# Kernel optimization log

Hardware: AMD Instinct MI355X
Metric: run time of the kernel (lower is better)

## Reference

```python
import jax, jax.numpy as jnp
import numpy as np

B, S, D, H = 2, 2048, 1024, 16
D_H = D // H  # 64


def setup_inputs() -> dict:
    key = jax.random.key(0)
    ks = jax.random.split(key, 12)
    inp = {
        "query": jax.random.normal(ks[0], (B, S, D), dtype=jnp.float32),
        "key":   jax.random.normal(ks[1], (B, S, D), dtype=jnp.float32),
        "value": jax.random.normal(ks[2], (B, S, D), dtype=jnp.float32),
        # causal 0/1 float mask, broadcastable to [B, H, Sq, Sk]; 1 = masked
        "mask":  jnp.broadcast_to(jnp.triu(jnp.ones((S, S), dtype=jnp.float32), k=1)[None, None], (B, 1, S, S)),
    }
    scale = 0.02
    inp["wq"] = jax.random.normal(ks[3], (D, D), dtype=jnp.float32) * scale
    inp["bq"] = jnp.zeros((D,), dtype=jnp.float32)
    inp["wk"] = jax.random.normal(ks[4], (D, D), dtype=jnp.float32) * scale
    inp["bk"] = jnp.zeros((D,), dtype=jnp.float32)
    inp["wv"] = jax.random.normal(ks[5], (D, D), dtype=jnp.float32) * scale
    inp["bv"] = jnp.zeros((D,), dtype=jnp.float32)
    inp["wff"] = jax.random.normal(ks[6], (D, D), dtype=jnp.float32) * scale
    inp["bff"] = jnp.zeros((D,), dtype=jnp.float32)
    return inp


def _split_head(x):
    # [B, S, D] -> [B, H, S, d_h]
    b, s, _ = x.shape
    return x.reshape(b, s, H, D_H).transpose(0, 2, 1, 3)


def reference(query, key, value, mask, wq, bq, wk, bk, wv, bv, wff, bff):
    # QKV projections (torch Linear: x @ W.T + b)
    q = _split_head(query @ wq.T + bq)
    k = _split_head(key @ wk.T + bk)
    v = _split_head(value @ wv.T + bv)
    # scaled dot-product attention
    scores = jnp.einsum("bhqd,bhkd->bhqk", q, k) / jnp.sqrt(jnp.float32(D_H))
    scores = scores + mask * (-1e9)
    attn = jax.nn.softmax(scores, axis=-1)
    out = jnp.einsum("bhqk,bhkd->bhqd", attn, v)
    # concat heads: [B, H, S, d_h] -> [B, S, D]
    out = out.transpose(0, 2, 1, 3).reshape(query.shape[0], query.shape[1], D)
    return out @ wff.T + bff
```

## Files before the change

### kernel.cpp

```cpp
#include <hip/hip_runtime.h>
#include <hip/hip_bf16.h>

#define B_  2
#define S_  2048
#define D_  1024
#define H_  16
#define DH_ 64
#define M_  (B_ * S_)

using bf16x8 = __attribute__((ext_vector_type(8))) short;
using s16x4  = __attribute__((ext_vector_type(4))) short;
using f32x4  = __attribute__((ext_vector_type(4))) float;

__device__ __forceinline__ bf16x8 ldg8(const __hip_bfloat16* p) {
    bf16x8 v;
    __builtin_memcpy(&v, p, 16);
    return v;
}
__device__ __forceinline__ bf16x8 lds8(const void* p) {
    bf16x8 v;
    __builtin_memcpy(&v, p, 16);
    return v;
}
__device__ __forceinline__ f32x4 lds4f(const void* p) {
    f32x4 v;
    __builtin_memcpy(&v, p, 16);
    return v;
}
__device__ __forceinline__ void gll16(const void* g, void* l) {
    __builtin_amdgcn_global_load_lds(
        (const __attribute__((address_space(1))) unsigned int*)g,
        (__attribute__((address_space(3))) unsigned int*)l,
        16, 0, 0);
}
__device__ __forceinline__ short bf16bits(float x) {
    __hip_bfloat16 hv = __float2bfloat16(x);
    short sv;
    __builtin_memcpy(&sv, &hv, 2);
    return sv;
}
__device__ __forceinline__ unsigned cvtpk(float lo, float hi) {
    unsigned r;
    asm("v_cvt_pk_bf16_f32 %0, %1, %2" : "=v"(r) : "v"(lo), "v"(hi));
    return r;
}

__global__ void cvt_w(const float* __restrict__ wq, const float* __restrict__ wk,
                      const float* __restrict__ wv, const float* __restrict__ wff,
                      __hip_bfloat16* __restrict__ Wq, __hip_bfloat16* __restrict__ Wk,
                      __hip_bfloat16* __restrict__ Wv, __hip_bfloat16* __restrict__ Wf) {
    const size_t e = (size_t)(blockIdx.x * 256 + threadIdx.x) * 8;
    const int i = (int)(e >> 20);
    const size_t off = e & (((size_t)1 << 20) - 1);
    const float* src = (i == 0) ? wq : (i == 1) ? wk : (i == 2) ? wv : wff;
    __hip_bfloat16* dst = (i == 0) ? Wq : (i == 1) ? Wk : (i == 2) ? Wv : Wf;
    float4 a, b;
    __builtin_memcpy(&a, src + off, 16);
    __builtin_memcpy(&b, src + off + 4, 16);
    __hip_bfloat16 h[8];
    h[0] = __float2bfloat16(a.x); h[1] = __float2bfloat16(a.y);
    h[2] = __float2bfloat16(a.z); h[3] = __float2bfloat16(a.w);
    h[4] = __float2bfloat16(b.x); h[5] = __float2bfloat16(b.y);
    h[6] = __float2bfloat16(b.z); h[7] = __float2bfloat16(b.w);
    __builtin_memcpy(dst + off, h, 16);
}

template<int MI, bool AF32>
__device__ __forceinline__
void gemm_body(const void* __restrict__ Ap,
               const __hip_bfloat16* __restrict__ W,
               const float* __restrict__ bias,
               void* __restrict__ out, int mode, float oscale,
               int row0, int col0) {
    constexpr int K  = D_;
    constexpr int N  = D_;
    constexpr int TM = MI * 32;
    constexpr int AB = AF32 ? 128 : 64;
    __shared__ __align__(16) char At[2][TM][AB];
    __shared__ __hip_bfloat16 Wt[2][128][32];

    const int tid = threadIdx.x;
    const int w   = tid >> 6;
    const int l   = tid & 63;
    const int lr  = l & 15;
    const int lg  = l >> 4;
    const int wr  = (w >> 1) * (MI * 16);
    const int wc  = (w & 1) * 64;

    const int srow4  = l >> 2;
    const int schk4  = l & 3;
    const int srow8  = l >> 3;
    const int schk8  = l & 7;

    f32x4 acc[MI][4] = {};

    auto STAGE = [&](int buf, int k0) {
        if (AF32) {
#pragma unroll
            for (int r = 0; r < TM / 32; ++r) {
                const int row = r * 32 + w * 8 + srow8;
                const int csw = (schk8 ^ (row & 7)) * 4;
                gll16((const float*)Ap + (size_t)(row0 + row) * K + k0 + csw,
                      &At[buf][r * 32 + w * 8][0]);
            }
        } else {
#pragma unroll
            for (int r = 0; r < TM / 64; ++r) {
                const int row = r * 64 + w * 16 + srow4;
                const int csw = (schk4 ^ (row & 3)) * 8;
                gll16((const __hip_bfloat16*)Ap + (size_t)(row0 + row) * K + k0 + csw,
                      &At[buf][r * 64 + w * 16][0]);
            }
        }
#pragma unroll
        for (int r = 0; r < 2; ++r) {
            const int row = r * 64 + w * 16 + srow4;
            const int csw = (schk4 ^ (row & 3)) * 8;
            gll16(W + (size_t)(col0 + row) * K + k0 + csw, &Wt[buf][r * 64 + w * 16][0]);
        }
    };

    STAGE(0, 0);
    int cur = 0;
    for (int k0 = 0; k0 < K; k0 += 32) {
        __syncthreads();
        if (k0 + 32 < K) STAGE(cur ^ 1, k0 + 32);
        bf16x8 af[MI], wf[4];
#pragma unroll
        for (int m = 0; m < MI; ++m) {
            const int arow = wr + m * 16 + lr;
            if (AF32) {
                const int c0 = (2 * lg) ^ (arow & 7);
                const int c1 = (2 * lg + 1) ^ (arow & 7);
                f32x4 a0 = lds4f(&At[cur][arow][c0 * 16]);
                f32x4 a1 = lds4f(&At[cur][arow][c1 * 16]);
                unsigned uu[4] = { cvtpk(a0[0], a0[1]), cvtpk(a0[2], a0[3]),
                                   cvtpk(a1[0], a1[1]), cvtpk(a1[2], a1[3]) };
                __builtin_memcpy(&af[m], uu, 16);
            } else {
                af[m] = lds8(&At[cur][arow][((lg ^ (arow & 3)) * 8) * 2]);
            }
        }
#pragma unroll
        for (int n = 0; n < 4; ++n) {
            const int wrow = wc + n * 16 + lr;
            wf[n] = lds8(&Wt[cur][wrow][(lg ^ (wrow & 3)) * 8]);
        }
#pragma unroll
        for (int m = 0; m < MI; ++m)
#pragma unroll
            for (int n = 0; n < 4; ++n)
                acc[m][n] = __builtin_amdgcn_mfma_f32_16x16x32_bf16(
                    af[m], wf[n], acc[m][n], 0, 0, 0);
        cur ^= 1;
    }

    float bv[4];
#pragma unroll
    for (int n = 0; n < 4; ++n) bv[n] = bias[col0 + wc + n * 16 + lr];

    if (mode == 1) {
#pragma unroll
        for (int m = 0; m < MI; ++m) {
            const int row_s = row0 + wr + m * 16 + lg * 4;
            const int bq = row_s >> 11, s0 = row_s & (S_ - 1);
#pragma unroll
            for (int n = 0; n < 4; ++n) {
                const int col = col0 + wc + n * 16 + lr;
                const int h = col >> 6, d = col & (DH_ - 1);
                s16x4 pk;
#pragma unroll
                for (int r = 0; r < 4; ++r) pk[r] = bf16bits(acc[m][n][r] + bv[n]);
                __builtin_memcpy(
                    (__hip_bfloat16*)out + ((size_t)((bq * H_ + h) * DH_) + d) * S_ + s0,
                    &pk, 8);
            }
        }
    } else {
#pragma unroll
        for (int m = 0; m < MI; ++m)
#pragma unroll
            for (int n = 0; n < 4; ++n)
#pragma unroll
                for (int r = 0; r < 4; ++r) {
                    const int row = row0 + wr + m * 16 + lg * 4 + r;
                    const int col = col0 + wc + n * 16 + lr;
                    const float v = acc[m][n][r] + bv[n];
                    if (mode == 0)
                        ((__hip_bfloat16*)out)[(size_t)row * N + col] =
                            __float2bfloat16(v * oscale);
                    else
                        ((float*)out)[(size_t)row * N + col] = v;
                }
    }
}

__global__ __launch_bounds__(256)
void gemm_qkv(const float* __restrict__ Xq, const float* __restrict__ Xk,
              const float* __restrict__ Xv, const __hip_bfloat16* __restrict__ Wq,
              const __hip_bfloat16* __restrict__ Wk, const __hip_bfloat16* __restrict__ Wv,
              const float* __restrict__ bq, const float* __restrict__ bk,
              const float* __restrict__ bv,
              __hip_bfloat16* __restrict__ Qp, __hip_bfloat16* __restrict__ Kp,
              __hip_bfloat16* __restrict__ Vt) {
    const int z = blockIdx.z;
    const void* A           = (z == 0) ? (const void*)Xq : (z == 1) ? (const void*)Xk : (const void*)Xv;
    const __hip_bfloat16* W = (z == 0) ? Wq : (z == 1) ? Wk : Wv;
    const float* bias       = (z == 0) ? bq : (z == 1) ? bk : bv;
    void* out               = (z == 0) ? (void*)Qp : (z == 1) ? (void*)Kp : (void*)Vt;
    const float osc = (z == 0) ? 0.125f * 1.4426950408889634f : 1.f;

    const int lin  = blockIdx.y * 8 + blockIdx.x;
    const int xcd  = lin & 7;
    const int idx  = lin >> 3;
    const int row0 = (xcd * 4 + (idx & 3)) * 128;
    const int col0 = (idx >> 2) * 128;

    gemm_body<4, true>(A, W, bias, out, (z == 2) ? 1 : 0, osc, row0, col0);
}

__global__ __launch_bounds__(256)
void gemm_ff(const __hip_bfloat16* __restrict__ A, const __hip_bfloat16* __restrict__ W,
             const float* __restrict__ bias, float* __restrict__ out) {
    const int lin  = blockIdx.y * 8 + blockIdx.x;
    const int xcd  = lin & 7;
    const int idx  = lin >> 3;
    const int row0 = (xcd * 8 + (idx & 7)) * 64;
    const int col0 = (idx >> 3) * 128;
    gemm_body<2, false>(A, W, bias, out, 2, 1.f, row0, col0);
}

__global__ __launch_bounds__(512)
void attn_fwd(const __hip_bfloat16* __restrict__ Qp,
              const __hip_bfloat16* __restrict__ Kp,
              const __hip_bfloat16* __restrict__ Vt,
              __hip_bfloat16* __restrict__ O) {
    __shared__ __hip_bfloat16 Kt[2][64][64];
    __shared__ __hip_bfloat16 Vs[2][64][64];
    __shared__ __hip_bfloat16 Pl[8][16][64];

    const int tid = threadIdx.x;
    const int w   = tid >> 6;
    const int l   = tid & 63;
    const int lr  = l & 15;
    const int lg  = l >> 4;

    const int raw = blockIdx.x;
    const int wg  = (raw & 7) * 64 + (raw >> 3);
    const int xcd = wg >> 6;
    const int loc = wg & 63;
    const int bhi = loc >> 4;
    const int prr = loc & 15;
    const int pr  = (bhi >= 2) ? (15 - prr) : prr;
    const int bh  = xcd * 4 + bhi;
    const int h   = bh & (H_ - 1);
    const int b   = bh >> 4;

    const int sub  = w >> 2;
    const int qb_s = sub ? (31 - pr) : pr;
    const int qw0  = qb_s * 64 + (w & 3) * 16;

    bf16x8 aq[2];
#pragma unroll
    for (int kc = 0; kc < 2; ++kc)
        aq[kc] = ldg8(Qp + (size_t)(b * S_ + qw0 + lr) * D_ + h * DH_ + kc * 32 + lg * 8);

    f32x4 o[4] = {};
    f32x4 rs4 = {};

    const int nkt_max = 32 - pr;

    const int srow   = l >> 3;
    const int schunk = l & 7;
    const int psw    = (lr & 7) << 4;

    auto STAGE = [&](int buf, int kt) {
        const int k0 = kt * 64;
        const int row = w * 8 + srow;
        const int csw = (schunk ^ (row & 7)) * 8;
        gll16(Kp + (size_t)(b * S_ + k0 + row) * D_ + h * DH_ + csw,
              &Kt[buf][w * 8][0]);
        gll16(Vt + ((size_t)((b * H_ + h) * DH_) + row) * S_ + k0 + csw,
              &Vs[buf][w * 8][0]);
    };

    char* prow = (char*)&Pl[w][lr][0];

    auto STEP = [&](int kt, int cur) {
        const int k0 = kt * 64;
        __syncthreads();
        if (kt + 1 < nkt_max) STAGE(cur ^ 1, kt + 1);

        if (kt <= qb_s) {
            f32x4 sc[4] = {};
            __builtin_amdgcn_s_setprio(1);
#pragma unroll
            for (int kk = 0; kk < 4; ++kk) {
                const int krow = kk * 16 + lr;
#pragma unroll
                for (int kc = 0; kc < 2; ++kc) {
                    bf16x8 kf = lds8(&Kt[cur][krow][((kc * 4 + lg) ^ (krow & 7)) * 8]);
                    sc[kk] = __builtin_amdgcn_mfma_f32_16x16x32_bf16(kf, aq[kc], sc[kk], 0, 0, 0);
                }
            }
            __builtin_amdgcn_s_setprio(0);

            const int qrow = qw0 + lr;
            if (kt == qb_s) {
#pragma unroll
                for (int kk = 0; kk < 4; ++kk) {
                    float pv[4];
#pragma unroll
                    for (int r = 0; r < 4; ++r) {
                        const int key = k0 + kk * 16 + lg * 4 + r;
                        pv[r] = (key > qrow) ? 0.f : exp2f(sc[kk][r]);
                        rs4[r] += pv[r];
                    }
                    unsigned uu[2] = { cvtpk(pv[0], pv[1]), cvtpk(pv[2], pv[3]) };
                    __builtin_memcpy(prow + ((kk * 32 + lg * 8) ^ psw), uu, 8);
                }
            } else {
#pragma unroll
                for (int kk = 0; kk < 4; ++kk) {
                    float pv[4];
#pragma unroll
                    for (int r = 0; r < 4; ++r) {
                        pv[r] = exp2f(sc[kk][r]);
                        rs4[r] += pv[r];
                    }
                    unsigned uu[2] = { cvtpk(pv[0], pv[1]), cvtpk(pv[2], pv[3]) };
                    __builtin_memcpy(prow + ((kk * 32 + lg * 8) ^ psw), uu, 8);
                }
            }

            bf16x8 pa[2];
#pragma unroll
            for (int kc = 0; kc < 2; ++kc)
                __builtin_memcpy(&pa[kc], prow + ((kc * 64 + lg * 16) ^ psw), 16);
            __builtin_amdgcn_s_setprio(1);
#pragma unroll
            for (int j = 0; j < 4; ++j) {
                const int vrow = j * 16 + lr;
#pragma unroll
                for (int kc = 0; kc < 2; ++kc) {
                    bf16x8 vf = lds8(&Vs[cur][vrow][((kc * 4 + lg) ^ (vrow & 7)) * 8]);
                    o[j] = __builtin_amdgcn_mfma_f32_16x16x32_bf16(pa[kc], vf, o[j], 0, 0, 0);
                }
            }
            __builtin_amdgcn_s_setprio(0);
        }
    };

    STAGE(0, 0);
    for (int kt = 0; kt < nkt_max; kt += 2) {
        STEP(kt, 0);
        if (kt + 1 < nkt_max) STEP(kt + 1, 1);
    }

    float rsf = rs4[0] + rs4[1] + rs4[2] + rs4[3];
    rsf += __shfl_xor(rsf, 16);
    rsf += __shfl_xor(rsf, 32);
#pragma unroll
    for (int r = 0; r < 4; ++r) {
        const float inv = 1.f / __shfl(rsf, 4 * lg + r);
        const int row = qw0 + 4 * lg + r;
#pragma unroll
        for (int j = 0; j < 4; ++j)
            O[((size_t)(b * S_ + row)) * D_ + h * DH_ + j * 16 + lr] =
                __float2bfloat16(o[j][r] * inv);
    }
}

extern "C" void kernel_launch(void* const* d_in, const int* in_sizes, int n_in,
                              void* d_out, int out_size, void* d_ws, size_t ws_size,
                              hipStream_t stream) {
    const float* q    = (const float*)d_in[0];
    const float* kin  = (const float*)d_in[1];
    const float* vin  = (const float*)d_in[2];
    const float* wq   = (const float*)d_in[4];
    const float* bq   = (const float*)d_in[5];
    const float* wk   = (const float*)d_in[6];
    const float* bk   = (const float*)d_in[7];
    const float* wv   = (const float*)d_in[8];
    const float* bv   = (const float*)d_in[9];
    const float* wff  = (const float*)d_in[10];
    const float* bff  = (const float*)d_in[11];

    char* ws = (char*)d_ws;
    const size_t MB = 1024 * 1024;
    __hip_bfloat16* Wqb = (__hip_bfloat16*)(ws + 24 * MB);
    __hip_bfloat16* Wkb = (__hip_bfloat16*)(ws + 26 * MB);
    __hip_bfloat16* Wvb = (__hip_bfloat16*)(ws + 28 * MB);
    __hip_bfloat16* Wfb = (__hip_bfloat16*)(ws + 30 * MB);
    __hip_bfloat16* Qp  = (__hip_bfloat16*)(ws + 32 * MB);
    __hip_bfloat16* Kp  = (__hip_bfloat16*)(ws + 40 * MB);
    __hip_bfloat16* Vt  = (__hip_bfloat16*)(ws + 48 * MB);
    __hip_bfloat16* Ob  = (__hip_bfloat16*)(ws + 56 * MB);

    cvt_w<<<2048, 256, 0, stream>>>(wq, wk, wv, wff, Wqb, Wkb, Wvb, Wfb);

    dim3 gq(8, 32, 3);
    gemm_qkv<<<gq, 256, 0, stream>>>(q, kin, vin, Wqb, Wkb, Wvb,
                                     bq, bk, bv, Qp, Kp, Vt);

    attn_fwd<<<512, 512, 0, stream>>>(Qp, Kp, Vt, Ob);

    dim3 gg(8, 64);
    gemm_ff<<<gg, 256, 0, stream>>>(Ob, Wfb, bff, (float*)d_out);
}
```

Baseline: 114.5 us.

## Balance causal attention work across warp groups with split-K on high query block

```diff
diff --git a/kernel.cpp b/kernel.cpp
--- a/kernel.cpp
+++ b/kernel.cpp
@@ -235,139 +235,164 @@
               const __hip_bfloat16* __restrict__ Kp,
               const __hip_bfloat16* __restrict__ Vt,
               __hip_bfloat16* __restrict__ O) {
-    __shared__ __hip_bfloat16 Kt[2][64][64];
-    __shared__ __hip_bfloat16 Vs[2][64][64];
-    __shared__ __hip_bfloat16 Pl[8][16][64];
+    __shared__ __hip_bfloat16 Kt[2][2][32][64];
+    __shared__ __hip_bfloat16 Vs[2][2][64][32];
+    __shared__ __hip_bfloat16 Pl[8][16][32];
 
     const int tid = threadIdx.x;
     const int w   = tid >> 6;
     const int l   = tid & 63;
     const int lr  = l & 15;
     const int lg  = l >> 4;
+    const int grp = w >> 2;
+    const int wi  = w & 3;
 
     const int raw = blockIdx.x;
     const int wg  = (raw & 7) * 64 + (raw >> 3);
-    const int xcd = wg >> 6;
-    const int loc = wg & 63;
-    const int bhi = loc >> 4;
-    const int prr = loc & 15;
-    const int pr  = (bhi >= 2) ? (15 - prr) : prr;
-    const int bh  = xcd * 4 + bhi;
+    const int bh  = wg >> 4;
+    const int pr  = wg & 15;
     const int h   = bh & (H_ - 1);
     const int b   = bh >> 4;
 
-    const int sub  = w >> 2;
-    const int qb_s = sub ? (31 - pr) : pr;
-    const int qw0  = qb_s * 64 + (w & 3) * 16;
-
-    bf16x8 aq[2];
-#pragma unroll
-    for (int kc = 0; kc < 2; ++kc)
-        aq[kc] = ldg8(Qp + (size_t)(b * S_ + qw0 + lr) * D_ + h * DH_ + kc * 32 + lg * 8);
-
-    f32x4 o[4] = {};
-    f32x4 rs4 = {};
-
-    const int nkt_max = 32 - pr;
-
-    const int srow   = l >> 3;
-    const int schunk = l & 7;
-    const int psw    = (lr & 7) << 4;
-
-    auto STAGE = [&](int buf, int kt) {
-        const int k0 = kt * 64;
-        const int row = w * 8 + srow;
-        const int csw = (schunk ^ (row & 7)) * 8;
-        gll16(Kp + (size_t)(b * S_ + k0 + row) * D_ + h * DH_ + csw,
-              &Kt[buf][w * 8][0]);
-        gll16(Vt + ((size_t)((b * H_ + h) * DH_) + row) * S_ + k0 + csw,
-              &Vs[buf][w * 8][0]);
+    const int qwL = pr * 64 + wi * 16;
+    const int qwH = (31 - pr) * 64 + wi * 16;
+    const int tL  = 2 * pr + 2;
+
+    const int psw = (lr & 3) << 4;
+
+    bf16x8 aqL[2], aqH[2];
+#pragma unroll
+    for (int kc = 0; kc < 2; ++kc) {
+        aqL[kc] = ldg8(Qp + (size_t)(b * S_ + qwL + lr) * D_ + h * DH_ + kc * 32 + lg * 8);
+        aqH[kc] = ldg8(Qp + (size_t)(b * S_ + qwH + lr) * D_ + h * DH_ + kc * 32 + lg * 8);
+    }
+
+    f32x4 oL[4] = {}, oH[4] = {};
+    f32x4 rsL4 = {}, rsH4 = {};
+
+    auto tile0 = [&](int s) { return (s < tL) ? s : (s + 31 - 2 * pr); };
+
+    auto STAGE = [&](int stream, int buf, int kt) {
+        const int k0 = kt * 32;
+        const int krow = wi * 8 + (l >> 3);
+        const int kcsw = ((l & 7) ^ (krow & 7)) * 8;
+        gll16(Kp + (size_t)(b * S_ + k0 + krow) * D_ + h * DH_ + kcsw,
+              &Kt[stream][buf][wi * 8][0]);
+        const int vrow = wi * 16 + (l >> 2);
+        const int vcsw = ((l & 3) ^ (vrow & 3)) * 8;
+        gll16(Vt + ((size_t)((b * H_ + h) * DH_) + vrow) * S_ + k0 + vcsw,
+              &Vs[stream][buf][wi * 16][0]);
     };
 
     char* prow = (char*)&Pl[w][lr][0];
 
-    auto STEP = [&](int kt, int cur) {
-        const int k0 = kt * 64;
+    auto UNIT = [&](int stream, int buf, int kt, const bf16x8 (&aq)[2],
+                    f32x4 (&o)[4], f32x4& rs4, int qw0) {
+        const int k0 = kt * 32;
+        f32x4 sc[2] = {};
+        __builtin_amdgcn_s_setprio(1);
+#pragma unroll
+        for (int kk = 0; kk < 2; ++kk) {
+            const int krow = kk * 16 + lr;
+#pragma unroll
+            for (int kc = 0; kc < 2; ++kc) {
+                bf16x8 kf = lds8(&Kt[stream][buf][krow][((kc * 4 + lg) ^ (krow & 7)) * 8]);
+                sc[kk] = __builtin_amdgcn_mfma_f32_16x16x32_bf16(kf, aq[kc], sc[kk], 0, 0, 0);
+            }
+        }
+        __builtin_amdgcn_s_setprio(0);
+
+        const int qrow = qw0 + lr;
+#pragma unroll
+        for (int kk = 0; kk < 2; ++kk) {
+            float pv[4];
+#pragma unroll
+            for (int r = 0; r < 4; ++r) {
+                const int key = k0 + kk * 16 + lg * 4 + r;
+                pv[r] = (key > qrow) ? 0.f : exp2f(sc[kk][r]);
+                rs4[r] += pv[r];
+            }
+            unsigned uu[2] = { cvtpk(pv[0], pv[1]), cvtpk(pv[2], pv[3]) };
+            __builtin_memcpy(prow + ((kk * 32 + lg * 8) ^ psw), uu, 8);
+        }
+
+        bf16x8 pa;
+        __builtin_memcpy(&pa, prow + ((lg * 16) ^ psw), 16);
+        __builtin_amdgcn_s_setprio(1);
+#pragma unroll
+        for (int j = 0; j < 4; ++j) {
+            const int vrow = j * 16 + lr;
+            bf16x8 vf = lds8(&Vs[stream][buf][vrow][(lg ^ (vrow & 3)) * 8]);
+            o[j] = __builtin_amdgcn_mfma_f32_16x16x32_bf16(pa, vf, o[j], 0, 0, 0);
+        }
+        __builtin_amdgcn_s_setprio(0);
+    };
+
+    if (grp == 0) STAGE(0, 0, tile0(0));
+    else          STAGE(1, 0, 0);
+
+    for (int s = 0; s < 33; ++s) {
+        const int buf = s & 1;
         __syncthreads();
-        if (kt + 1 < nkt_max) STAGE(cur ^ 1, kt + 1);
-
-        if (kt <= qb_s) {
-            f32x4 sc[4] = {};
-            __builtin_amdgcn_s_setprio(1);
-#pragma unroll
-            for (int kk = 0; kk < 4; ++kk) {
-                const int krow = kk * 16 + lr;
-#pragma unroll
-                for (int kc = 0; kc < 2; ++kc) {
-                    bf16x8 kf = lds8(&Kt[cur][krow][((kc * 4 + lg) ^ (krow & 7)) * 8]);
-                    sc[kk] = __builtin_amdgcn_mfma_f32_16x16x32_bf16(kf, aq[kc], sc[kk], 0, 0, 0);
-                }
-            }
-            __builtin_amdgcn_s_setprio(0);
-
-            const int qrow = qw0 + lr;
-            if (kt == qb_s) {
-#pragma unroll
-                for (int kk = 0; kk < 4; ++kk) {
-                    float pv[4];
-#pragma unroll
-                    for (int r = 0; r < 4; ++r) {
-                        const int key = k0 + kk * 16 + lg * 4 + r;
-                        pv[r] = (key > qrow) ? 0.f : exp2f(sc[kk][r]);
-                        rs4[r] += pv[r];
-                    }
-                    unsigned uu[2] = { cvtpk(pv[0], pv[1]), cvtpk(pv[2], pv[3]) };
-                    __builtin_memcpy(prow + ((kk * 32 + lg * 8) ^ psw), uu, 8);
-                }
-            } else {
-#pragma unroll
-                for (int kk = 0; kk < 4; ++kk) {
-                    float pv[4];
-#pragma unroll
-                    for (int r = 0; r < 4; ++r) {
-                        pv[r] = exp2f(sc[kk][r]);
-                        rs4[r] += pv[r];
-                    }
-                    unsigned uu[2] = { cvtpk(pv[0], pv[1]), cvtpk(pv[2], pv[3]) };
-                    __builtin_memcpy(prow + ((kk * 32 + lg * 8) ^ psw), uu, 8);
-                }
-            }
-
-            bf16x8 pa[2];
-#pragma unroll
-            for (int kc = 0; kc < 2; ++kc)
-                __builtin_memcpy(&pa[kc], prow + ((kc * 64 + lg * 16) ^ psw), 16);
-            __builtin_amdgcn_s_setprio(1);
-#pragma unroll
-            for (int j = 0; j < 4; ++j) {
-                const int vrow = j * 16 + lr;
-#pragma unroll
-                for (int kc = 0; kc < 2; ++kc) {
-                    bf16x8 vf = lds8(&Vs[cur][vrow][((kc * 4 + lg) ^ (vrow & 7)) * 8]);
-                    o[j] = __builtin_amdgcn_mfma_f32_16x16x32_bf16(pa[kc], vf, o[j], 0, 0, 0);
-                }
-            }
-            __builtin_amdgcn_s_setprio(0);
-        }
+        if (s + 1 < 33) {
+            if (grp == 0) STAGE(0, buf ^ 1, tile0(s + 1));
+            else          STAGE(1, buf ^ 1, s + 1);
+        }
+        if (grp == 0) {
+            if (s < tL) UNIT(0, buf, s, aqL, oL, rsL4, qwL);
+            else        UNIT(0, buf, s + 31 - 2 * pr, aqH, oH, rsH4, qwH);
+        } else {
+            UNIT(1, buf, s, aqH, oH, rsH4, qwH);
+        }
+    }
+
+    auto rsum = [&](const f32x4& v) {
+        float x = v[0] + v[1] + v[2] + v[3];
+        x += __shfl_xor(x, 16);
+        x += __shfl_xor(x, 32);
+        return x;
     };
 
-    STAGE(0, 0);
-    for (int kt = 0; kt < nkt_max; kt += 2) {
-        STEP(kt, 0);
-        if (kt + 1 < nkt_max) STEP(kt + 1, 1);
-    }
-
-    float rsf = rs4[0] + rs4[1] + rs4[2] + rs4[3];
-    rsf += __shfl_xor(rsf, 16);
-    rsf += __shfl_xor(rsf, 32);
-#pragma unroll
-    for (int r = 0; r < 4; ++r) {
-        const float inv = 1.f / __shfl(rsf, 4 * lg + r);
-        const int row = qw0 + 4 * lg + r;
+    float* Ox = (float*)&Kt[0][0][0][0];
+    float* Rx = (float*)&Vs[0][0][0][0];
+
+    __syncthreads();
+    if (grp == 1) {
+        const float rsf = rsum(rsH4);
 #pragma unroll
         for (int j = 0; j < 4; ++j)
-            O[((size_t)(b * S_ + row)) * D_ + h * DH_ + j * 16 + lr] =
-                __float2bfloat16(o[j][r] * inv);
+#pragma unroll
+            for (int r = 0; r < 4; ++r)
+                Ox[(wi * 16 + 4 * lg + r) * 64 + j * 16 + lr] = oH[j][r];
+        if (l < 16) Rx[wi * 16 + lr] = rsf;
+    }
+    __syncthreads();
+    if (grp == 0) {
+        const float rsfL = rsum(rsL4);
+#pragma unroll
+        for (int r = 0; r < 4; ++r) {
+            const float inv = 1.f / __shfl(rsfL, 4 * lg + r);
+            const int row = qwL + 4 * lg + r;
+#pragma unroll
+            for (int j = 0; j < 4; ++j)
+                O[((size_t)(b * S_ + row)) * D_ + h * DH_ + j * 16 + lr] =
+                    __float2bfloat16(oL[j][r] * inv);
+        }
+        const float tot = rsum(rsH4) + Rx[wi * 16 + lr];
+#pragma unroll
+        for (int j = 0; j < 4; ++j)
+#pragma unroll
+            for (int r = 0; r < 4; ++r)
+                oH[j][r] += Ox[(wi * 16 + 4 * lg + r) * 64 + j * 16 + lr];
+#pragma unroll
+        for (int r = 0; r < 4; ++r) {
+            const float inv = 1.f / __shfl(tot, 4 * lg + r);
+            const int row = qwH + 4 * lg + r;
+#pragma unroll
+            for (int j = 0; j < 4; ++j)
+                O[((size_t)(b * S_ + row)) * D_ + h * DH_ + j * 16 + lr] =
+                    __float2bfloat16(oH[j][r] * inv);
+        }
     }
 }
 
```

Result: slower. 118.9 us (+3.9%).

## Stage 128-key K/V tiles per barrier in causal attention kernel

Applied to the files above, without the earlier changes.

```diff
diff --git a/kernel.cpp b/kernel.cpp
--- a/kernel.cpp
+++ b/kernel.cpp
@@ -235,8 +235,8 @@
               const __hip_bfloat16* __restrict__ Kp,
               const __hip_bfloat16* __restrict__ Vt,
               __hip_bfloat16* __restrict__ O) {
-    __shared__ __hip_bfloat16 Kt[2][64][64];
-    __shared__ __hip_bfloat16 Vs[2][64][64];
+    __shared__ __hip_bfloat16 Kt[2][128][64];
+    __shared__ __hip_bfloat16 Vs[2][64][128];
     __shared__ __hip_bfloat16 Pl[8][16][64];
 
     const int tid = threadIdx.x;
@@ -247,12 +247,11 @@
 
     const int raw = blockIdx.x;
     const int wg  = (raw & 7) * 64 + (raw >> 3);
-    const int xcd = wg >> 6;
     const int loc = wg & 63;
     const int bhi = loc >> 4;
     const int prr = loc & 15;
     const int pr  = (bhi >= 2) ? (15 - prr) : prr;
-    const int bh  = xcd * 4 + bhi;
+    const int bh  = (wg >> 6) * 4 + bhi;
     const int h   = bh & (H_ - 1);
     const int b   = bh >> 4;
 
@@ -268,93 +267,86 @@
     f32x4 o[4] = {};
     f32x4 rs4 = {};
 
-    const int nkt_max = 32 - pr;
-
-    const int srow   = l >> 3;
-    const int schunk = l & 7;
-    const int psw    = (lr & 7) << 4;
-
-    auto STAGE = [&](int buf, int kt) {
-        const int k0 = kt * 64;
-        const int row = w * 8 + srow;
-        const int csw = (schunk ^ (row & 7)) * 8;
-        gll16(Kp + (size_t)(b * S_ + k0 + row) * D_ + h * DH_ + csw,
-              &Kt[buf][w * 8][0]);
-        gll16(Vt + ((size_t)((b * H_ + h) * DH_) + row) * S_ + k0 + csw,
-              &Vs[buf][w * 8][0]);
+    const int nt = (33 - pr) >> 1;
+    const int psw = (lr & 7) << 4;
+
+    auto STAGE = [&](int buf, int t) {
+        const int k0 = t * 128;
+#pragma unroll
+        for (int r = 0; r < 2; ++r) {
+            const int krow = w * 16 + r * 8 + (l >> 3);
+            const int kcsw = ((l & 7) ^ (krow & 7)) * 8;
+            gll16(Kp + (size_t)(b * S_ + k0 + krow) * D_ + h * DH_ + kcsw,
+                  &Kt[buf][w * 16 + r * 8][0]);
+        }
+#pragma unroll
+        for (int r = 0; r < 2; ++r) {
+            const int vrow = w * 8 + r * 4 + (l >> 4);
+            const int vcsw = ((l & 15) ^ (vrow & 15)) * 8;
+            gll16(Vt + ((size_t)((b * H_ + h) * DH_) + vrow) * S_ + k0 + vcsw,
+                  &Vs[buf][w * 8 + r * 4][0]);
+        }
     };
 
     char* prow = (char*)&Pl[w][lr][0];
 
-    auto STEP = [&](int kt, int cur) {
-        const int k0 = kt * 64;
+    auto UNIT = [&](int buf, int u, int half) {
+        const int k0 = u * 64;
+        f32x4 sc[4] = {};
+        __builtin_amdgcn_s_setprio(1);
+#pragma unroll
+        for (int kk = 0; kk < 4; ++kk) {
+            const int krow = half * 64 + kk * 16 + lr;
+#pragma unroll
+            for (int kc = 0; kc < 2; ++kc) {
+                bf16x8 kf = lds8(&Kt[buf][krow][((kc * 4 + lg) ^ (krow & 7)) * 8]);
+                sc[kk] = __builtin_amdgcn_mfma_f32_16x16x32_bf16(kf, aq[kc], sc[kk], 0, 0, 0);
+            }
+        }
+        __builtin_amdgcn_s_setprio(0);
+
+        const int qrow = qw0 + lr;
+#pragma unroll
+        for (int kk = 0; kk < 4; ++kk) {
+            float pv[4];
+#pragma unroll
+            for (int r = 0; r < 4; ++r) {
+                const int key = k0 + kk * 16 + lg * 4 + r;
+                pv[r] = (key > qrow) ? 0.f : exp2f(sc[kk][r]);
+                rs4[r] += pv[r];
+            }
+            unsigned uu[2] = { cvtpk(pv[0], pv[1]), cvtpk(pv[2], pv[3]) };
+            __builtin_memcpy(prow + ((kk * 32 + lg * 8) ^ psw), uu, 8);
+        }
+
+        bf16x8 pa[2];
+#pragma unroll
+        for (int kc = 0; kc < 2; ++kc)
+            __builtin_memcpy(&pa[kc], prow + ((kc * 64 + lg * 16) ^ psw), 16);
+        __builtin_amdgcn_s_setprio(1);
+#pragma unroll
+        for (int j = 0; j < 4; ++j) {
+            const int vrow = j * 16 + lr;
+#pragma unroll
+            for (int kc = 0; kc < 2; ++kc) {
+                const int chunk = (half * 8 + kc * 4 + lg) ^ (vrow & 15);
+                bf16x8 vf = lds8(&Vs[buf][vrow][chunk * 8]);
+                o[j] = __builtin_amdgcn_mfma_f32_16x16x32_bf16(pa[kc], vf, o[j], 0, 0, 0);
+            }
+        }
+        __builtin_amdgcn_s_setprio(0);
+    };
+
+    STAGE(0, 0);
+    for (int t = 0; t < nt; ++t) {
+        const int buf = t & 1;
         __syncthreads();
-        if (kt + 1 < nkt_max) STAGE(cur ^ 1, kt + 1);
-
-        if (kt <= qb_s) {
-            f32x4 sc[4] = {};
-            __builtin_amdgcn_s_setprio(1);
-#pragma unroll
-            for (int kk = 0; kk < 4; ++kk) {
-                const int krow = kk * 16 + lr;
-#pragma unroll
-                for (int kc = 0; kc < 2; ++kc) {
-                    bf16x8 kf = lds8(&Kt[cur][krow][((kc * 4 + lg) ^ (krow & 7)) * 8]);
-                    sc[kk] = __builtin_amdgcn_mfma_f32_16x16x32_bf16(kf, aq[kc], sc[kk], 0, 0, 0);
-                }
-            }
-            __builtin_amdgcn_s_setprio(0);
-
-            const int qrow = qw0 + lr;
-            if (kt == qb_s) {
-#pragma unroll
-                for (int kk = 0; kk < 4; ++kk) {
-                    float pv[4];
-#pragma unroll
-                    for (int r = 0; r < 4; ++r) {
-                        const int key = k0 + kk * 16 + lg * 4 + r;
-                        pv[r] = (key > qrow) ? 0.f : exp2f(sc[kk][r]);
-                        rs4[r] += pv[r];
-                    }
-                    unsigned uu[2] = { cvtpk(pv[0], pv[1]), cvtpk(pv[2], pv[3]) };
-                    __builtin_memcpy(prow + ((kk * 32 + lg * 8) ^ psw), uu, 8);
-                }
-            } else {
-#pragma unroll
-                for (int kk = 0; kk < 4; ++kk) {
-                    float pv[4];
-#pragma unroll
-                    for (int r = 0; r < 4; ++r) {
-                        pv[r] = exp2f(sc[kk][r]);
-                        rs4[r] += pv[r];
-                    }
-                    unsigned uu[2] = { cvtpk(pv[0], pv[1]), cvtpk(pv[2], pv[3]) };
-                    __builtin_memcpy(prow + ((kk * 32 + lg * 8) ^ psw), uu, 8);
-                }
-            }
-
-            bf16x8 pa[2];
-#pragma unroll
-            for (int kc = 0; kc < 2; ++kc)
-                __builtin_memcpy(&pa[kc], prow + ((kc * 64 + lg * 16) ^ psw), 16);
-            __builtin_amdgcn_s_setprio(1);
-#pragma unroll
-            for (int j = 0; j < 4; ++j) {
-                const int vrow = j * 16 + lr;
-#pragma unroll
-                for (int kc = 0; kc < 2; ++kc) {
-                    bf16x8 vf = lds8(&Vs[cur][vrow][((kc * 4 + lg) ^ (vrow & 7)) * 8]);
-                    o[j] = __builtin_amdgcn_mfma_f32_16x16x32_bf16(pa[kc], vf, o[j], 0, 0, 0);
-                }
-            }
-            __builtin_amdgcn_s_setprio(0);
-        }
-    };
-
-    STAGE(0, 0);
-    for (int kt = 0; kt < nkt_max; kt += 2) {
-        STEP(kt, 0);
-        if (kt + 1 < nkt_max) STEP(kt + 1, 1);
+        if (t + 1 < nt) STAGE(buf ^ 1, t + 1);
+#pragma unroll
+        for (int half = 0; half < 2; ++half) {
+            const int u = 2 * t + half;
+            if (u <= qb_s) UNIT(buf, u, half);
+        }
     }
 
     float rsf = rs4[0] + rs4[1] + rs4[2] + rs4[3];
```

After: 118.5 us. 3.5% more time.

## Deepen attention K/V staging to four buffers and software-pipeline QK ahead of softmax-PV

Applied to the files above, without the earlier changes.

```diff
diff --git a/kernel.cpp b/kernel.cpp
--- a/kernel.cpp
+++ b/kernel.cpp
@@ -235,8 +235,8 @@
               const __hip_bfloat16* __restrict__ Kp,
               const __hip_bfloat16* __restrict__ Vt,
               __hip_bfloat16* __restrict__ O) {
-    __shared__ __hip_bfloat16 Kt[2][64][64];
-    __shared__ __hip_bfloat16 Vs[2][64][64];
+    __shared__ __hip_bfloat16 Kt[4][64][64];
+    __shared__ __hip_bfloat16 Vs[4][64][64];
     __shared__ __hip_bfloat16 Pl[8][16][64];
 
     const int tid = threadIdx.x;
@@ -268,7 +268,7 @@
     f32x4 o[4] = {};
     f32x4 rs4 = {};
 
-    const int nkt_max = 32 - pr;
+    const int nkt = 32 - pr;
 
     const int srow   = l >> 3;
     const int schunk = l & 7;
@@ -286,75 +286,94 @@
 
     char* prow = (char*)&Pl[w][lr][0];
 
-    auto STEP = [&](int kt, int cur) {
+    auto QK = [&](int buf, f32x4 (&sc)[4]) {
+        __builtin_amdgcn_s_setprio(1);
+#pragma unroll
+        for (int kk = 0; kk < 4; ++kk) {
+            const int krow = kk * 16 + lr;
+#pragma unroll
+            for (int kc = 0; kc < 2; ++kc) {
+                bf16x8 kf = lds8(&Kt[buf][krow][((kc * 4 + lg) ^ (krow & 7)) * 8]);
+                sc[kk] = __builtin_amdgcn_mfma_f32_16x16x32_bf16(kf, aq[kc], sc[kk], 0, 0, 0);
+            }
+        }
+        __builtin_amdgcn_s_setprio(0);
+    };
+
+    auto SMPV = [&](int buf, int kt, f32x4 (&sc)[4]) {
         const int k0 = kt * 64;
-        __syncthreads();
-        if (kt + 1 < nkt_max) STAGE(cur ^ 1, kt + 1);
-
-        if (kt <= qb_s) {
-            f32x4 sc[4] = {};
-            __builtin_amdgcn_s_setprio(1);
+        const int qrow = qw0 + lr;
+        if (kt == qb_s) {
 #pragma unroll
             for (int kk = 0; kk < 4; ++kk) {
-                const int krow = kk * 16 + lr;
-#pragma unroll
-                for (int kc = 0; kc < 2; ++kc) {
-                    bf16x8 kf = lds8(&Kt[cur][krow][((kc * 4 + lg) ^ (krow & 7)) * 8]);
-                    sc[kk] = __builtin_amdgcn_mfma_f32_16x16x32_bf16(kf, aq[kc], sc[kk], 0, 0, 0);
+                float pv[4];
+#pragma unroll
+                for (int r = 0; r < 4; ++r) {
+                    const int key = k0 + kk * 16 + lg * 4 + r;
+                    pv[r] = (key > qrow) ? 0.f : exp2f(sc[kk][r]);
+                    rs4[r] += pv[r];
                 }
-            }
-            __builtin_amdgcn_s_setprio(0);
-
-            const int qrow = qw0 + lr;
-            if (kt == qb_s) {
-#pragma unroll
-                for (int kk = 0; kk < 4; ++kk) {
-                    float pv[4];
-#pragma unroll
-                    for (int r = 0; r < 4; ++r) {
-                        const int key = k0 + kk * 16 + lg * 4 + r;
-                        pv[r] = (key > qrow) ? 0.f : exp2f(sc[kk][r]);
-                        rs4[r] += pv[r];
-                    }
-                    unsigned uu[2] = { cvtpk(pv[0], pv[1]), cvtpk(pv[2], pv[3]) };
-                    __builtin_memcpy(prow + ((kk * 32 + lg * 8) ^ psw), uu, 8);
+                unsigned uu[2] = { cvtpk(pv[0], pv[1]), cvtpk(pv[2], pv[3]) };
+                __builtin_memcpy(prow + ((kk * 32 + lg * 8) ^ psw), uu, 8);
+            }
+        } else {
+#pragma unroll
+            for (int kk = 0; kk < 4; ++kk) {
+                float pv[4];
+#pragma unroll
+                for (int r = 0; r < 4; ++r) {
+                    pv[r] = exp2f(sc[kk][r]);
+                    rs4[r] += pv[r];
                 }
-            } else {
-#pragma unroll
-                for (int kk = 0; kk < 4; ++kk) {
-                    float pv[4];
-#pragma unroll
-                    for (int r = 0; r < 4; ++r) {
-                        pv[r] = exp2f(sc[kk][r]);
-                        rs4[r] += pv[r];
-                    }
-                    unsigned uu[2] = { cvtpk(pv[0], pv[1]), cvtpk(pv[2], pv[3]) };
-                    __builtin_memcpy(prow + ((kk * 32 + lg * 8) ^ psw), uu, 8);
-                }
-            }
-
-            bf16x8 pa[2];
-#pragma unroll
-            for (int kc = 0; kc < 2; ++kc)
-                __builtin_memcpy(&pa[kc], prow + ((kc * 64 + lg * 16) ^ psw), 16);
-            __builtin_amdgcn_s_setprio(1);
-#pragma unroll
-            for (int j = 0; j < 4; ++j) {
-                const int vrow = j * 16 + lr;
-#pragma unroll
-                for (int kc = 0; kc < 2; ++kc) {
-                    bf16x8 vf = lds8(&Vs[cur][vrow][((kc * 4 + lg) ^ (vrow & 7)) * 8]);
-                    o[j] = __builtin_amdgcn_mfma_f32_16x16x32_bf16(pa[kc], vf, o[j], 0, 0, 0);
-                }
-            }
-            __builtin_amdgcn_s_setprio(0);
-        }
+                unsigned uu[2] = { cvtpk(pv[0], pv[1]), cvtpk(pv[2], pv[3]) };
+                __builtin_memcpy(prow + ((kk * 32 + lg * 8) ^ psw), uu, 8);
+            }
+        }
+
+        bf16x8 pa[2];
+#pragma unroll
+        for (int kc = 0; kc < 2; ++kc)
+            __builtin_memcpy(&pa[kc], prow + ((kc * 64 + lg * 16) ^ psw), 16);
+        __builtin_amdgcn_s_setprio(1);
+#pragma unroll
+        for (int j = 0; j < 4; ++j) {
+            const int vrow = j * 16 + lr;
+#pragma unroll
+            for (int kc = 0; kc < 2; ++kc) {
+                bf16x8 vf = lds8(&Vs[buf][vrow][((kc * 4 + lg) ^ (vrow & 7)) * 8]);
+                o[j] = __builtin_amdgcn_mfma_f32_16x16x32_bf16(pa[kc], vf, o[j], 0, 0, 0);
+            }
+        }
+        __builtin_amdgcn_s_setprio(0);
     };
 
-    STAGE(0, 0);
-    for (int kt = 0; kt < nkt_max; kt += 2) {
-        STEP(kt, 0);
-        if (kt + 1 < nkt_max) STEP(kt + 1, 1);
+    f32x4 scA[4] = {}, scB[4] = {};
+
+    auto ITER = [&](int t, int bc, f32x4 (&scC)[4], f32x4 (&scN)[4]) {
+        if (t + 2 < nkt) { asm volatile("s_waitcnt vmcnt(2)" ::: "memory"); }
+        else             { asm volatile("s_waitcnt vmcnt(0)" ::: "memory"); }
+        __builtin_amdgcn_s_barrier();
+        __builtin_amdgcn_sched_barrier(0);
+        if (t + 3 < nkt) STAGE((bc + 3) & 3, t + 3);
+        if (t + 1 <= qb_s) {
+#pragma unroll
+            for (int i = 0; i < 4; ++i) scN[i] = f32x4{0.f, 0.f, 0.f, 0.f};
+            QK((bc + 1) & 3, scN);
+        }
+        if (t <= qb_s) SMPV(bc, t, scC);
+    };
+
+    STAGE(0, 0); STAGE(1, 1); STAGE(2, 2);
+    asm volatile("s_waitcnt vmcnt(4)" ::: "memory");
+    __builtin_amdgcn_s_barrier();
+    __builtin_amdgcn_sched_barrier(0);
+    QK(0, scA);
+
+    for (int t = 0; t < nkt; t += 4) {
+        ITER(t + 0, 0, scA, scB);
+        if (t + 1 < nkt) ITER(t + 1, 1, scB, scA);
+        if (t + 2 < nkt) ITER(t + 2, 2, scA, scB);
+        if (t + 3 < nkt) ITER(t + 3, 3, scB, scA);
     }
 
     float rsf = rs4[0] + rs4[1] + rs4[2] + rs4[3];
```

Measured after the change: 112.5 us (median of 2 runs). About the same (-1.7%).
